# Kernel tuning notes

Measured on AMD Instinct MI355X. Metric: run time of the kernel, lower is better.

Reference implementation:

```python
import jax, jax.numpy as jnp
import numpy as np

N_NODES = 100000
N_EDGES = 3200000
IN_DIM = 256
HIDDEN = 128
OUT_DIM = 64


def setup_inputs() -> dict:
    key = jax.random.key(0)
    k = jax.random.split(key, 6)
    x = jax.random.normal(k[0], (N_NODES, IN_DIM), dtype=jnp.float32)
    adj_vals = jax.random.uniform(k[1], (N_EDGES,), dtype=jnp.float32)
    # glorot init as in the original
    s1 = np.sqrt(6.0 / (IN_DIM + HIDDEN)).astype(np.float32)
    s2 = np.sqrt(6.0 / (HIDDEN + OUT_DIM)).astype(np.float32)
    w1 = jax.random.uniform(k[2], (IN_DIM, HIDDEN), dtype=jnp.float32, minval=-s1, maxval=s1)
    w2 = jax.random.uniform(k[3], (HIDDEN, OUT_DIM), dtype=jnp.float32, minval=-s2, maxval=s2)
    edge_src = jax.random.randint(k[4], (N_EDGES,), 0, N_NODES, dtype=jnp.int32)
    edge_dst = jax.random.randint(k[5], (N_EDGES,), 0, N_NODES, dtype=jnp.int32)
    return {"x": x, "adj_vals": adj_vals, "w1": w1, "w2": w2,
            "edge_src": edge_src, "edge_dst": edge_dst}


def _spmm(adj_vals, edge_src, edge_dst, h, n_nodes):
    """Sparse adjacency (COO) times dense matrix: out[d] = sum_e vals[e]*h[src[e]]."""
    msgs = adj_vals[:, None] * h[edge_src]  # [E, D] gather + scale
    return jax.ops.segment_sum(msgs, edge_dst, num_segments=n_nodes)


def reference(x, adj_vals, w1, w2, edge_src, edge_dst):
    # Layer 1: pre_sup = X @ W1; support = A @ pre_sup; relu
    h = jax.nn.relu(_spmm(adj_vals, edge_src, edge_dst, x @ w1, N_NODES))
    # Layer 2: identity activation -> logits
    logits = _spmm(adj_vals, edge_src, edge_dst, h @ w2, N_NODES)
    return logits
```

## Files before the change

### kernel.cpp

```cpp
#include <hip/hip_runtime.h>

#define N_NODES 100000
#define N_EDGES 3200000
#define IN_DIM 256
#define HIDDEN 128
#define OUT_DIM 64

#define NBUCK 782
#define CHUNK 3072
#define NPT (CHUNK / 256)
#define NPB ((N_EDGES + CHUNK - 1) / CHUNK)
#define BCAP 6144
#define CURSTRIDE 32
#define NCG 13
#define CGBITS 13
#define MAXCH 92

typedef unsigned int uint32;
typedef unsigned short ushort16;

typedef short short8 __attribute__((ext_vector_type(8)));
typedef float f32x4 __attribute__((ext_vector_type(4)));

__device__ __forceinline__ ushort16 f2bf(float f) {
    uint32 u = __float_as_uint(f);
    u += 0x7fffu + ((u >> 16) & 1u);
    return (ushort16)(u >> 16);
}

__device__ __forceinline__ void splitbf(float f, unsigned short& hi, unsigned short& lo) {
    uint32 u = __float_as_uint(f);
    uint32 r = u + 0x7fffu + ((u >> 16) & 1u);
    hi = (unsigned short)(r >> 16);
    float hf = __uint_as_float((r >> 16) << 16);
    float res = f - hf;
    uint32 v = __float_as_uint(res);
    lo = (unsigned short)((v + 0x7fffu + ((v >> 16) & 1u)) >> 16);
}


__global__ __launch_bounds__(256)
void hist_bucket(const int* __restrict__ edst, int* __restrict__ bcnt, int E) {
    __shared__ int h[NBUCK];
    for (int b = threadIdx.x; b < NBUCK; b += 256) h[b] = 0;
    __syncthreads();
    for (int i = blockIdx.x * 256 + threadIdx.x; i < E; i += gridDim.x * 256)
        atomicAdd(&h[edst[i] >> 7], 1);
    __syncthreads();
    for (int b = threadIdx.x; b < NBUCK; b += 256) {
        int c = h[b];
        if (c) atomicAdd(&bcnt[b], c);
    }
}


__global__ __launch_bounds__(256)
void bucket_scan(const int* __restrict__ bcnt, int* __restrict__ bptr,
                 int* __restrict__ cursor, int* __restrict__ gcur,
                 int* __restrict__ row_ptr, int E) {
    __shared__ int st[256];
    int tid = threadIdx.x;
    int v4[4];
    int s0 = 0;
#pragma unroll
    for (int k = 0; k < 4; k++) {
        int b = tid * 4 + k;
        v4[k] = (b < NBUCK) ? bcnt[b] : 0;
        s0 += v4[k];
    }
    st[tid] = s0;
    __syncthreads();
    for (int off = 1; off < 256; off <<= 1) {
        int t = (tid >= off) ? st[tid - off] : 0;
        __syncthreads();
        st[tid] += t;
        __syncthreads();
    }
    int run = st[tid] - s0;
    if ((tid & 15) == 0 && (tid >> 4) < NCG) gcur[(tid >> 4) * CURSTRIDE] = run;
#pragma unroll
    for (int k = 0; k < 4; k++) {
        int b = tid * 4 + k;
        if (b < NBUCK) { bptr[b] = run; cursor[b * CURSTRIDE] = run; }
        run += v4[k];
    }
    if (tid == 255) bptr[NBUCK] = run;
    if (tid == 0) row_ptr[N_NODES] = E;
}


__global__ __launch_bounds__(512)
void bucket_to_csr(const int* __restrict__ bptr, int2* __restrict__ part,
                   int* __restrict__ row_ptr) {
    __shared__ int2 se[BCAP];
    __shared__ int rcnt[128];
    __shared__ int rcur[128];
    int tid = threadIdx.x;
    int b = blockIdx.x;
    int s = bptr[b], e = bptr[b + 1];
    int cnt = min(e - s, BCAP);

    if (tid < 128) rcnt[tid] = 0;
    __syncthreads();
    for (int j = tid; j < cnt; j += 512) {
        int2 p = part[s + j];
        se[j] = p;
        atomicAdd(&rcnt[p.x >> 17], 1);
    }
    __syncthreads();

    int v = (tid < 128) ? rcnt[tid] : 0;
    if (tid < 128) rcur[tid] = v;
    __syncthreads();
    for (int off = 1; off < 128; off <<= 1) {
        int t = 0;
        if (tid < 128 && tid >= off) t = rcur[tid - off];
        __syncthreads();
        if (tid < 128 && tid >= off) rcur[tid] += t;
        __syncthreads();
    }
    if (tid < 128) {
        int excl = rcur[tid] - v;
        rcur[tid] = excl;
        int row = b * 128 + tid;
        if (row < N_NODES) row_ptr[row] = s + excl;
    }
    __syncthreads();

    for (int j = tid; j < cnt; j += 512) {
        int2 p = se[j];
        int r = p.x >> 17;
        int pos = atomicAdd(&rcur[r], 1);
        part[s + pos] = make_int2(p.x & 0x1FFFF, p.y);
    }
}


__global__ __launch_bounds__(256)
void splitw_kernel(const float* __restrict__ w1, const float* __restrict__ w2,
                   unsigned short* __restrict__ w1f_hi, unsigned short* __restrict__ w1f_lo,
                   unsigned short* __restrict__ w2f_hi, unsigned short* __restrict__ w2f_lo) {
    const int W1_SLOTS = (IN_DIM / 32) * (HIDDEN / 16) * 64;
    const int W2_SLOTS = (HIDDEN / 32) * (OUT_DIM / 16) * 64;
    int g = blockIdx.x * 256 + threadIdx.x;
    if (g < W1_SLOTS) {
        int lane = g & 63;
        int rest = g >> 6;
        int nfrag = rest & 7;
        int kblk = rest >> 3;
        int n = nfrag * 16 + (lane & 15);
        int k0 = kblk * 32 + (lane >> 4) * 8;
#pragma unroll
        for (int j = 0; j < 8; j++) {
            unsigned short h, l;
            splitbf(w1[(size_t)(k0 + j) * HIDDEN + n], h, l);
            w1f_hi[(size_t)g * 8 + j] = h;
            w1f_lo[(size_t)g * 8 + j] = l;
        }
    } else if (g < W1_SLOTS + W2_SLOTS) {
        int g2 = g - W1_SLOTS;
        int lane = g2 & 63;
        int rest = g2 >> 6;
        int nfrag = rest & 3;
        int kblk = rest >> 2;
        int n = nfrag * 16 + (lane & 15);
        int k0 = kblk * 32 + (lane >> 4) * 8;
#pragma unroll
        for (int j = 0; j < 8; j++) {
            unsigned short h, l;
            splitbf(w2[(size_t)(k0 + j) * OUT_DIM + n], h, l);
            w2f_hi[(size_t)g2 * 8 + j] = h;
            w2f_lo[(size_t)g2 * 8 + j] = l;
        }
    }
}


template <int K, int BN>
__device__ __forceinline__ void gemm_body(int bx, char* smem, const float* __restrict__ A,
                                          const unsigned short* __restrict__ Bf_hi,
                                          const unsigned short* __restrict__ Bf_lo,
                                          ushort16* __restrict__ C, int M) {
    constexpr int BM = 128, BK = 64;
    constexpr int NF = BN / 32;
    unsigned short* Ah = (unsigned short*)smem;
    unsigned short* Al = (unsigned short*)(smem + BM * BK * 2);

    int tid = threadIdx.x;
    int wid = tid >> 6, lane = tid & 63;
    int wr = wid >> 1, wc = wid & 1;
    int rowBase = bx * BM;
    int r = lane & 15, kg = lane >> 4;
    int swzmask = (lane & 7) << 4;

    f32x4 zero = {0.f, 0.f, 0.f, 0.f};
    f32x4 acc[4][NF];
#pragma unroll
    for (int m = 0; m < 4; m++)
#pragma unroll
        for (int n = 0; n < NF; n++) acc[m][n] = zero;

    int sk4 = (tid & 15) * 4;
    int sm0 = tid >> 4;

    for (int k0 = 0; k0 < K; k0 += BK) {
#pragma unroll
        for (int i = 0; i < 8; i++) {
            int m = sm0 + i * 16;
            int row = rowBase + m;
            float4 f = make_float4(0.f, 0.f, 0.f, 0.f);
            if (row < M) f = *(const float4*)(A + (size_t)row * K + k0 + sk4);
            ushort4 h, l;
            splitbf(f.x, h.x, l.x);
            splitbf(f.y, h.y, l.y);
            splitbf(f.z, h.z, l.z);
            splitbf(f.w, h.w, l.w);
            int bo = (m * BK + sk4) * 2;
            int swz = bo ^ ((m & 7) << 4);
            *(ushort4*)((char*)Ah + swz) = h;
            *(ushort4*)((char*)Al + swz) = l;
        }
        __syncthreads();

#pragma unroll
        for (int kk = 0; kk < BK / 32; kk++) {
            short8 ah[4], al[4];
            int abase = (wr * 64 + r) * (BK * 2) + kk * 64 + kg * 16;
#pragma unroll
            for (int m = 0; m < 4; m++) {
                int swz = (abase + m * (16 * BK * 2)) ^ swzmask;
                ah[m] = *(const short8*)((const char*)Ah + swz);
                al[m] = *(const short8*)((const char*)Al + swz);
            }
            short8 bh[NF], bl[NF];
            int kblk = (k0 >> 5) + kk;
#pragma unroll
            for (int n = 0; n < NF; n++) {
                int nf = wc * NF + n;
                size_t off = ((size_t)(kblk * (BN / 16) + nf) * 64 + lane) * 8;
                bh[n] = *(const short8*)(Bf_hi + off);
                bl[n] = *(const short8*)(Bf_lo + off);
            }
#pragma unroll
            for (int m = 0; m < 4; m++)
#pragma unroll
                for (int n = 0; n < NF; n++) {
                    acc[m][n] = __builtin_amdgcn_mfma_f32_16x16x32_bf16(ah[m], bh[n], acc[m][n], 0, 0, 0);
                    acc[m][n] = __builtin_amdgcn_mfma_f32_16x16x32_bf16(ah[m], bl[n], acc[m][n], 0, 0, 0);
                    acc[m][n] = __builtin_amdgcn_mfma_f32_16x16x32_bf16(al[m], bh[n], acc[m][n], 0, 0, 0);
                }
        }
        __syncthreads();
    }

#pragma unroll
    for (int m = 0; m < 4; m++) {
        int row0 = rowBase + wr * 64 + m * 16 + kg * 4;
#pragma unroll
        for (int j = 0; j < 4; j++) {
            int row = row0 + j;
            if (row < M) {
#pragma unroll
                for (int n = 0; n < NF; n++) {
                    int col = wc * (BN / 2) + n * 16 + r;
                    C[(size_t)row * BN + col] = f2bf(acc[m][n][j]);
                }
            }
        }
    }
}

template <int K, int BN>
__launch_bounds__(256)
__global__ void gemm_mfma(const float* __restrict__ A,
                          const unsigned short* __restrict__ Bf_hi,
                          const unsigned short* __restrict__ Bf_lo,
                          ushort16* __restrict__ C, int M) {
    __shared__ __align__(16) char smem[32768];
    gemm_body<K, BN>(blockIdx.x, smem, A, Bf_hi, Bf_lo, C, M);
}


__launch_bounds__(256)
__global__ void partition_gemm1(const int* __restrict__ esrc, const int* __restrict__ edst,
                                const float* __restrict__ evals, int* __restrict__ gcur,
                                int2* __restrict__ part2, int E,
                                const float* __restrict__ A,
                                const unsigned short* __restrict__ w1f_hi,
                                const unsigned short* __restrict__ w1f_lo,
                                ushort16* __restrict__ pre1, int M) {
    __shared__ __align__(16) char smem[32768];
    if (blockIdx.x >= NPB) {
        gemm_body<IN_DIM, HIDDEN>(blockIdx.x - NPB, smem, A, w1f_hi, w1f_lo, pre1, M);
        return;
    }
    int2* sbp = (int2*)smem;
    unsigned char* sbg = (unsigned char*)(smem + 24576);
    int* hist = (int*)(smem + 27648);
    int* lst  = (int*)(smem + 27712);
    int* bpos = (int*)(smem + 27776);

    int tid = threadIdx.x;
    long base = (long)blockIdx.x * CHUNK;
    int cnt = (int)min((long)CHUNK, (long)E - base);

    if (tid < NCG) hist[tid] = 0;
    __syncthreads();

    int d[NPT], sv[NPT]; float vv[NPT];
#pragma unroll
    for (int k = 0; k < NPT; k++) {
        int j = tid + k * 256;
        d[k] = -1;
        if (j < cnt) {
            d[k]  = edst[base + j];
            sv[k] = esrc[base + j];
            vv[k] = evals[base + j];
            atomicAdd(&hist[d[k] >> CGBITS], 1);
        }
    }
    __syncthreads();

    if (tid == 0) {
        int run = 0;
#pragma unroll
        for (int g = 0; g < NCG; g++) { lst[g] = run; run += hist[g]; }
    }
    __syncthreads();

    if (tid < NCG) {
        int c = hist[tid];
        int g = c ? atomicAdd(&gcur[tid * CURSTRIDE], c) : 0;
        bpos[tid] = g - lst[tid];
        hist[tid] = lst[tid];
    }
    __syncthreads();

#pragma unroll
    for (int k = 0; k < NPT; k++) {
        int j = tid + k * 256;
        if (j < cnt) {
            int dd = d[k], g = dd >> CGBITS;
            int pos = atomicAdd(&hist[g], 1);
            sbg[pos] = (unsigned char)g;
            sbp[pos] = make_int2(sv[k] | ((dd & 8191) << 17), __float_as_int(vv[k]));
        }
    }
    __syncthreads();

    for (int j = tid; j < cnt; j += 256)
        part2[bpos[sbg[j]] + j] = sbp[j];
}


__global__ __launch_bounds__(256)
void pass2_kernel(const int2* __restrict__ part2, const int* __restrict__ bptr,
                  int* __restrict__ cursor, int2* __restrict__ part) {
    __shared__ __align__(16) int2 sbp[CHUNK];
    __shared__ unsigned char sbb[CHUNK];
    __shared__ int hist[64], lst[64], bpos[64];
    int tid = threadIdx.x;
    int g = blockIdx.x / MAXCH;
    int c = blockIdx.x % MAXCH;
    int gs = bptr[min(64 * g, NBUCK)];
    int ge = bptr[min(64 * (g + 1), NBUCK)];
    int base = gs + c * CHUNK;
    if (base >= ge) return;
    int cnt = min(CHUNK, ge - base);
    int b0 = g * 64;

    if (tid < 64) hist[tid] = 0;
    __syncthreads();

    int lb[NPT]; int2 pp[NPT];
#pragma unroll
    for (int k = 0; k < NPT; k++) {
        int j = tid + k * 256;
        lb[k] = -1;
        if (j < cnt) {
            pp[k] = part2[base + j];
            int dst = (g << CGBITS) | ((uint32)pp[k].x >> 17);
            lb[k] = (dst >> 7) - b0;
            atomicAdd(&hist[lb[k]], 1);
        }
    }
    __syncthreads();

    if (tid < 64) {
        int cc = hist[tid];
        int sum = cc;
#pragma unroll
        for (int off = 1; off < 64; off <<= 1) {
            int up = __shfl_up(sum, off);
            if (tid >= off) sum += up;
        }
        lst[tid] = sum - cc;
    }
    __syncthreads();

    if (tid < 64) {
        int cc = hist[tid];
        int gp = cc ? atomicAdd(&cursor[(b0 + tid) * CURSTRIDE], cc) : 0;
        bpos[tid] = gp - lst[tid];
        hist[tid] = lst[tid];
    }
    __syncthreads();

#pragma unroll
    for (int k = 0; k < NPT; k++) {
        int j = tid + k * 256;
        if (j < cnt) {
            int b = lb[k];
            int pos = atomicAdd(&hist[b], 1);
            sbb[pos] = (unsigned char)b;
            int dst = (g << CGBITS) | ((uint32)pp[k].x >> 17);
            sbp[pos] = make_int2((pp[k].x & 0x1FFFF) | ((dst & 127) << 17), pp[k].y);
        }
    }
    __syncthreads();

    for (int j = tid; j < cnt; j += 256)
        part[bpos[sbb[j]] + j] = sbp[j];
}


template <int D, bool RELU>
__launch_bounds__(256)
__global__ void spmm_kernel(const ushort16* __restrict__ feat, const int2* __restrict__ csr_pair,
                            const int* __restrict__ row_ptr, float* __restrict__ out, int n) {
    constexpr int LPR = D * 2 / 16;
    constexpr int EPG = 64 / LPR;
    constexpr int DEPTH = (D == 128) ? 8 : 4;
    int wid = threadIdx.x >> 6;
    int lane = threadIdx.x & 63;
    int row = blockIdx.x * 4 + wid;
    if (row >= n) return;
    int s = row_ptr[row], e = row_ptr[row + 1];

    int sub = lane / LPR;
    int slot = lane % LPR;
    const char* fbase = (const char*)feat + slot * 16;

    float acc[8];
#pragma unroll
    for (int j = 0; j < 8; j++) acc[j] = 0.f;

    for (int i = s; i < e; i += DEPTH * EPG) {
        int2 p[DEPTH]; float v[DEPTH]; uint4 u[DEPTH];
#pragma unroll
        for (int q = 0; q < DEPTH; q++) {
            int ii = i + q * EPG + sub;
            p[q] = csr_pair[min(ii, e - 1)];
            v[q] = (ii < e) ? __int_as_float(p[q].y) : 0.f;
        }
#pragma unroll
        for (int q = 0; q < DEPTH; q++)
            u[q] = *(const uint4*)(fbase + (size_t)p[q].x * (D * 2));
#pragma unroll
        for (int q = 0; q < DEPTH; q++) {
#pragma unroll
            for (int t = 0; t < 4; t++) {
                uint32 w = (&u[q].x)[t];
                acc[2 * t]     += v[q] * __uint_as_float(w << 16);
                acc[2 * t + 1] += v[q] * __uint_as_float(w & 0xffff0000u);
            }
        }
    }

#pragma unroll
    for (int m = LPR; m < 64; m <<= 1) {
#pragma unroll
        for (int j = 0; j < 8; j++) acc[j] += __shfl_xor(acc[j], m);
    }

    if (RELU) {
#pragma unroll
        for (int j = 0; j < 8; j++) acc[j] = acc[j] > 0.f ? acc[j] : 0.f;
    }

    if (lane < LPR) {
        float4* o = (float4*)(out + (size_t)row * D + slot * 8);
        o[0] = make_float4(acc[0], acc[1], acc[2], acc[3]);
        o[1] = make_float4(acc[4], acc[5], acc[6], acc[7]);
    }
}


extern "C" void kernel_launch(void* const* d_in, const int* in_sizes, int n_in,
                              void* d_out, int out_size, void* d_ws, size_t ws_size,
                              hipStream_t stream) {
    const float* x    = (const float*)d_in[0];
    const float* adj  = (const float*)d_in[1];
    const float* w1   = (const float*)d_in[2];
    const float* w2   = (const float*)d_in[3];
    const int*   esrc = (const int*)d_in[4];
    const int*   edst = (const int*)d_in[5];
    float* out = (float*)d_out;

    const int N = N_NODES;
    const int E = N_EDGES;

    char* ws = (char*)d_ws;
    size_t off = 0;
    auto take = [&](size_t bytes) -> char* {
        char* p = ws + off;
        off = (off + bytes + 255) & ~(size_t)255;
        return p;
    };
    int*      bcnt    = (int*)take((size_t)NBUCK * 4);
    int*      bptr    = (int*)take((size_t)(NBUCK + 1) * 4);
    int*      cursor  = (int*)take((size_t)NBUCK * CURSTRIDE * 4);
    int*      gcur    = (int*)take((size_t)NCG * CURSTRIDE * 4);
    int*      row_ptr = (int*)take((size_t)(N + 1) * 4);
    int2*     part    = (int2*)take((size_t)E * 8);
    int2*     part2   = (int2*)take((size_t)E * 8);
    ushort16* pre1    = (ushort16*)take((size_t)N * HIDDEN * 2);
    ushort16* pre2    = (ushort16*)take((size_t)N * OUT_DIM * 2);
    float*    h       = (float*)take((size_t)N * HIDDEN * 4);
    unsigned short* w1f_hi = (unsigned short*)take((size_t)HIDDEN * IN_DIM * 2);
    unsigned short* w1f_lo = (unsigned short*)take((size_t)HIDDEN * IN_DIM * 2);
    unsigned short* w2f_hi = (unsigned short*)take((size_t)OUT_DIM * HIDDEN * 2);
    unsigned short* w2f_lo = (unsigned short*)take((size_t)OUT_DIM * HIDDEN * 2);

    splitw_kernel<<<20, 256, 0, stream>>>(w1, w2, w1f_hi, w1f_lo, w2f_hi, w2f_lo);

    hipMemsetAsync(bcnt, 0, (size_t)NBUCK * 4, stream);
    hist_bucket<<<1024, 256, 0, stream>>>(edst, bcnt, E);
    bucket_scan<<<1, 256, 0, stream>>>(bcnt, bptr, cursor, gcur, row_ptr, E);

    partition_gemm1<<<NPB + (N_NODES + 127) / 128, 256, 0, stream>>>(
        esrc, edst, adj, gcur, part2, E, x, w1f_hi, w1f_lo, pre1, N);

    pass2_kernel<<<NCG * MAXCH, 256, 0, stream>>>(part2, bptr, cursor, part);

    bucket_to_csr<<<NBUCK, 512, 0, stream>>>(bptr, part, row_ptr);

    spmm_kernel<HIDDEN, true><<<(N + 3) / 4, 256, 0, stream>>>(pre1, part, row_ptr, h, N);

    gemm_mfma<HIDDEN, OUT_DIM><<<(N + 127) / 128, 256, 0, stream>>>(h, w2f_hi, w2f_lo, pre2, N);
    spmm_kernel<OUT_DIM, false><<<(N + 3) / 4, 256, 0, stream>>>(pre2, part, row_ptr, out, N);
}
```

Baseline: 488.1 us.

## Precompute per-chunk group offsets to make partition deterministic and avoid global atomics

The histogram kernel now runs one block per partition chunk and records per-chunk counts for each coarse group. A new scan kernel prefix-sums these counts per group to give each chunk a fixed output base, replacing the global atomic cursors in the partition pass. The partition kernel also uses per-wavefront shared histograms so the scatter is stable and shared-atomic contention drops. This adds one extra small kernel launch and some extra global traffic for the chunk tables.

```diff
diff --git a/kernel.cpp b/kernel.cpp
--- a/kernel.cpp
+++ b/kernel.cpp
@@ -40,24 +40,33 @@
 
 
 __global__ __launch_bounds__(256)
-void hist_bucket(const int* __restrict__ edst, int* __restrict__ bcnt, int E) {
+void hist_bucket(const int* __restrict__ edst, int* __restrict__ bcnt,
+                 int* __restrict__ chunk_hist, int E) {
     __shared__ int h[NBUCK];
-    for (int b = threadIdx.x; b < NBUCK; b += 256) h[b] = 0;
-    __syncthreads();
-    for (int i = blockIdx.x * 256 + threadIdx.x; i < E; i += gridDim.x * 256)
-        atomicAdd(&h[edst[i] >> 7], 1);
-    __syncthreads();
-    for (int b = threadIdx.x; b < NBUCK; b += 256) {
+    int tid = threadIdx.x;
+    long base = (long)blockIdx.x * CHUNK;
+    int cnt = (int)min((long)CHUNK, (long)E - base);
+    for (int b = tid; b < NBUCK; b += 256) h[b] = 0;
+    __syncthreads();
+    for (int j = tid; j < cnt; j += 256)
+        atomicAdd(&h[edst[base + j] >> 7], 1);
+    __syncthreads();
+    for (int b = tid; b < NBUCK; b += 256) {
         int c = h[b];
         if (c) atomicAdd(&bcnt[b], c);
     }
+    if (tid < NCG) {
+        int b0 = tid * 64, b1 = min(b0 + 64, NBUCK);
+        int s = 0;
+        for (int b = b0; b < b1; b++) s += h[b];
+        chunk_hist[blockIdx.x * 16 + tid] = s;
+    }
 }
 
 
 __global__ __launch_bounds__(256)
 void bucket_scan(const int* __restrict__ bcnt, int* __restrict__ bptr,
-                 int* __restrict__ cursor, int* __restrict__ gcur,
-                 int* __restrict__ row_ptr, int E) {
+                 int* __restrict__ cursor, int* __restrict__ row_ptr, int E) {
     __shared__ int st[256];
     int tid = threadIdx.x;
     int v4[4];
@@ -77,7 +86,6 @@
         __syncthreads();
     }
     int run = st[tid] - s0;
-    if ((tid & 15) == 0 && (tid >> 4) < NCG) gcur[(tid >> 4) * CURSTRIDE] = run;
 #pragma unroll
     for (int k = 0; k < 4; k++) {
         int b = tid * 4 + k;
@@ -86,6 +94,34 @@
     }
     if (tid == 255) bptr[NBUCK] = run;
     if (tid == 0) row_ptr[N_NODES] = E;
+}
+
+
+__global__ __launch_bounds__(256)
+void scan_chunks(const int* __restrict__ chunk_hist, const int* __restrict__ bptr,
+                 int* __restrict__ chunk_base) {
+    __shared__ int st[256];
+    int g = blockIdx.x;
+    int tid = threadIdx.x;
+    int carry = bptr[min(64 * g, NBUCK)];
+    for (int t0 = 0; t0 < NPB; t0 += 256) {
+        int c = t0 + tid;
+        int v = (c < NPB) ? chunk_hist[c * 16 + g] : 0;
+        st[tid] = v;
+        __syncthreads();
+        int sum = v;
+        for (int off = 1; off < 256; off <<= 1) {
+            int t = (tid >= off) ? st[tid - off] : 0;
+            __syncthreads();
+            sum += t;
+            st[tid] = sum;
+            __syncthreads();
+        }
+        if (c < NPB) chunk_base[c * 16 + g] = carry + sum - v;
+        int tot = st[255];
+        __syncthreads();
+        carry += tot;
+    }
 }
 
 
@@ -283,7 +319,8 @@
 
 __launch_bounds__(256)
 __global__ void partition_gemm1(const int* __restrict__ esrc, const int* __restrict__ edst,
-                                const float* __restrict__ evals, int* __restrict__ gcur,
+                                const float* __restrict__ evals,
+                                const int* __restrict__ chunk_base,
                                 int2* __restrict__ part2, int E,
                                 const float* __restrict__ A,
                                 const unsigned short* __restrict__ w1f_hi,
@@ -296,15 +333,17 @@
     }
     int2* sbp = (int2*)smem;
     unsigned char* sbg = (unsigned char*)(smem + 24576);
-    int* hist = (int*)(smem + 27648);
-    int* lst  = (int*)(smem + 27712);
-    int* bpos = (int*)(smem + 27776);
-
-    int tid = threadIdx.x;
+    int* whist = (int*)(smem + 27648);
+    int* tmp   = (int*)(smem + 27904);
+    int* lst   = (int*)(smem + 27968);
+    int* bpos  = (int*)(smem + 28032);
+
+    int tid = threadIdx.x;
+    int wid = tid >> 6;
     long base = (long)blockIdx.x * CHUNK;
     int cnt = (int)min((long)CHUNK, (long)E - base);
 
-    if (tid < NCG) hist[tid] = 0;
+    if (tid < 64) whist[tid] = 0;
     __syncthreads();
 
     int d[NPT], sv[NPT]; float vv[NPT];
@@ -316,34 +355,39 @@
             d[k]  = edst[base + j];
             sv[k] = esrc[base + j];
             vv[k] = evals[base + j];
-            atomicAdd(&hist[d[k] >> CGBITS], 1);
-        }
-    }
-    __syncthreads();
-
+            atomicAdd(&whist[wid * 16 + (d[k] >> CGBITS)], 1);
+        }
+    }
+    __syncthreads();
+
+    if (tid < NCG)
+        tmp[tid] = whist[tid] + whist[16 + tid] + whist[32 + tid] + whist[48 + tid];
+    __syncthreads();
     if (tid == 0) {
         int run = 0;
 #pragma unroll
-        for (int g = 0; g < NCG; g++) { lst[g] = run; run += hist[g]; }
-    }
-    __syncthreads();
-
+        for (int g = 0; g < NCG; g++) { lst[g] = run; run += tmp[g]; }
+    }
+    __syncthreads();
     if (tid < NCG) {
-        int c = hist[tid];
-        int g = c ? atomicAdd(&gcur[tid * CURSTRIDE], c) : 0;
-        bpos[tid] = g - lst[tid];
-        hist[tid] = lst[tid];
+        int g = tid;
+        int c0 = whist[g], c1 = whist[16 + g], c2 = whist[32 + g];
+        int l = lst[g];
+        whist[g]      = l;
+        whist[16 + g] = l + c0;
+        whist[32 + g] = l + c0 + c1;
+        whist[48 + g] = l + c0 + c1 + c2;
+        bpos[g] = chunk_base[blockIdx.x * 16 + g] - l;
     }
     __syncthreads();
 
 #pragma unroll
     for (int k = 0; k < NPT; k++) {
-        int j = tid + k * 256;
-        if (j < cnt) {
-            int dd = d[k], g = dd >> CGBITS;
-            int pos = atomicAdd(&hist[g], 1);
+        if (d[k] >= 0) {
+            int g = d[k] >> CGBITS;
+            int pos = atomicAdd(&whist[wid * 16 + g], 1);
             sbg[pos] = (unsigned char)g;
-            sbp[pos] = make_int2(sv[k] | ((dd & 8191) << 17), __float_as_int(vv[k]));
+            sbp[pos] = make_int2(sv[k] | ((d[k] & 8191) << 17), __float_as_int(vv[k]));
         }
     }
     __syncthreads();
@@ -507,16 +551,17 @@
         off = (off + bytes + 255) & ~(size_t)255;
         return p;
     };
-    int*      bcnt    = (int*)take((size_t)NBUCK * 4);
-    int*      bptr    = (int*)take((size_t)(NBUCK + 1) * 4);
-    int*      cursor  = (int*)take((size_t)NBUCK * CURSTRIDE * 4);
-    int*      gcur    = (int*)take((size_t)NCG * CURSTRIDE * 4);
-    int*      row_ptr = (int*)take((size_t)(N + 1) * 4);
-    int2*     part    = (int2*)take((size_t)E * 8);
-    int2*     part2   = (int2*)take((size_t)E * 8);
-    ushort16* pre1    = (ushort16*)take((size_t)N * HIDDEN * 2);
-    ushort16* pre2    = (ushort16*)take((size_t)N * OUT_DIM * 2);
-    float*    h       = (float*)take((size_t)N * HIDDEN * 4);
+    int*      bcnt       = (int*)take((size_t)NBUCK * 4);
+    int*      bptr       = (int*)take((size_t)(NBUCK + 1) * 4);
+    int*      cursor     = (int*)take((size_t)NBUCK * CURSTRIDE * 4);
+    int*      chunk_hist = (int*)take((size_t)NPB * 16 * 4);
+    int*      chunk_base = (int*)take((size_t)NPB * 16 * 4);
+    int*      row_ptr    = (int*)take((size_t)(N + 1) * 4);
+    int2*     part       = (int2*)take((size_t)E * 8);
+    int2*     part2      = (int2*)take((size_t)E * 8);
+    ushort16* pre1       = (ushort16*)take((size_t)N * HIDDEN * 2);
+    ushort16* pre2       = (ushort16*)take((size_t)N * OUT_DIM * 2);
+    float*    h          = (float*)take((size_t)N * HIDDEN * 4);
     unsigned short* w1f_hi = (unsigned short*)take((size_t)HIDDEN * IN_DIM * 2);
     unsigned short* w1f_lo = (unsigned short*)take((size_t)HIDDEN * IN_DIM * 2);
     unsigned short* w2f_hi = (unsigned short*)take((size_t)OUT_DIM * HIDDEN * 2);
@@ -525,11 +570,12 @@
     splitw_kernel<<<20, 256, 0, stream>>>(w1, w2, w1f_hi, w1f_lo, w2f_hi, w2f_lo);
 
     hipMemsetAsync(bcnt, 0, (size_t)NBUCK * 4, stream);
-    hist_bucket<<<1024, 256, 0, stream>>>(edst, bcnt, E);
-    bucket_scan<<<1, 256, 0, stream>>>(bcnt, bptr, cursor, gcur, row_ptr, E);
+    hist_bucket<<<NPB, 256, 0, stream>>>(edst, bcnt, chunk_hist, E);
+    bucket_scan<<<1, 256, 0, stream>>>(bcnt, bptr, cursor, row_ptr, E);
+    scan_chunks<<<NCG, 256, 0, stream>>>(chunk_hist, bptr, chunk_base);
 
     partition_gemm1<<<NPB + (N_NODES + 127) / 128, 256, 0, stream>>>(
-        esrc, edst, adj, gcur, part2, E, x, w1f_hi, w1f_lo, pre1, N);
+        esrc, edst, adj, chunk_base, part2, E, x, w1f_hi, w1f_lo, pre1, N);
 
     pass2_kernel<<<NCG * MAXCH, 256, 0, stream>>>(part2, bptr, cursor, part);
 
```

After: 491.5 us. About the same (+0.7%).
